# Kernel tuning notes

Hardware: AMD Instinct MI355X
Metric: run time of the kernel (lower is better)

Reference implementation:

```python
import jax, jax.numpy as jnp
import numpy as np
import math

MUL = 64
N_NODES = 20000
N_EDGES = 160000
NUM_SPECIES = 5
N_BASIS = 8
AVG_NEIGH = 8.0
SOFT_NORM_MAX = 1.0e5
# (l_in, l_filter, l_out) tensor-product paths with triangle ineq. + parity (l_in+l_f+l_out even), l_f <= 2
PATHS = [(0,0,0),(0,1,1),(0,2,2),(1,0,1),(1,1,0),(1,1,2),(1,2,1),(2,0,2),(2,1,1),(2,2,0),(2,2,2)]
SQ_PATHS = [(0,0,0),(0,1,1),(0,2,2),(1,1,0),(1,1,2),(1,2,1),(2,2,0),(2,2,2)]

def _clebsch(j1,m1,j2,m2,j3,m3):
    if m1 + m2 != m3:
        return 0.0
    f = math.factorial
    pref = math.sqrt((2*j3+1)*f(j3+j1-j2)*f(j3-j1+j2)*f(j1+j2-j3)/f(j1+j2+j3+1))
    pref *= math.sqrt(f(j3+m3)*f(j3-m3)*f(j1-m1)*f(j1+m1)*f(j2-m2)*f(j2+m2))
    s = 0.0
    for k in range(j1+j2-j3+1):
        d = [k, j1+j2-j3-k, j1-m1-k, j2+m2-k, j3-j2+m1+k, j3-j1-m2+k]
        if min(d) < 0:
            continue
        den = 1.0
        for q in d:
            den *= f(q)
        s += (-1)**k/den
    return pref*s

def _u_real(l):
    # complex->real spherical harmonic change of basis, rows = real m (-l..l)
    U = np.zeros((2*l+1, 2*l+1), dtype=np.complex128)
    U[l, l] = 1.0
    r2 = math.sqrt(2.0)
    for m in range(1, l+1):
        U[l+m, l+m] = (-1)**m/r2
        U[l+m, l-m] = 1.0/r2
        U[l-m, l-m] = 1j/r2
        U[l-m, l+m] = -1j*(-1)**m/r2
    return U

def _cg_real(l1,l2,l3):
    Cc = np.zeros((2*l1+1, 2*l2+1, 2*l3+1), dtype=np.complex128)
    for m1 in range(-l1, l1+1):
        for m2 in range(-l2, l2+1):
            m3 = m1 + m2
            if abs(m3) <= l3:
                Cc[m1+l1, m2+l2, m3+l3] = _clebsch(l1,m1,l2,m2,l3,m3)
    R = np.einsum('ai,bj,ck,ijk->abc', _u_real(l1), _u_real(l2), _u_real(l3).conj(), Cc)
    Rr, Ri = R.real, R.imag
    R = Rr if np.linalg.norm(Rr) >= np.linalg.norm(Ri) else Ri
    return jnp.asarray((R/np.linalg.norm(R)).astype(np.float32))

CG = {p: _cg_real(*p) for p in sorted(set(PATHS) | set(SQ_PATHS))}

def _sh(dirs):
    # real spherical harmonics (component normalization) of unit vectors, l=0,1,2
    x, y, z = dirs[:, 0], dirs[:, 1], dirs[:, 2]
    Y0 = jnp.ones_like(x)[:, None]
    Y1 = jnp.sqrt(3.0)*jnp.stack([y, z, x], axis=1)
    Y2 = jnp.stack([jnp.sqrt(15.0)*x*y, jnp.sqrt(15.0)*y*z,
                    jnp.sqrt(5.0)/2*(3*z*z - 1.0), jnp.sqrt(15.0)*x*z,
                    jnp.sqrt(15.0)/2*(x*x - y*y)], axis=1)
    return [Y0, Y1, Y2]

def _split(feats):
    # [.., 576] -> [[.., 64, 1], [.., 64, 3], [.., 64, 5]]
    out, s = [], 0
    for l in range(3):
        d = 2*l + 1
        out.append(feats[..., s:s+MUL*d].reshape(feats.shape[:-1] + (MUL, d)))
        s += MUL*d
    return out

def _merge(blocks):
    return jnp.concatenate([b.reshape(b.shape[:-2] + (-1,)) for b in blocks], axis=-1)

def _sus(x):
    return jnp.where(x > 0, jnp.exp(-1.0/jnp.where(x > 0, x, 1.0)), 0.0)

def _forward(vectors, node_feats, W_up, W_skip, M1, M2, M3, W_out0, W_out1, W_out2, W_down,
             node_specie, senders, receivers):
    n_node = node_feats.shape[0]
    nf = _split(node_feats)
    # self connection: species-indexed linear (skip_tp)
    Wn = W_skip[node_specie]  # [N, 3, mul, mul]
    skip = [jnp.einsum('nui,nuv->nvi', nf[l], Wn[:, l]) / np.sqrt(MUL) for l in range(3)]
    # linear_up then gather sender features
    up = [jnp.einsum('nui,uv->nvi', nf[l], W_up[l]) / np.sqrt(MUL) for l in range(3)]
    msg = [u[senders] for u in up]  # per-edge messages
    # radial MLP -> per-edge tensor-product path weights
    lengths = jnp.linalg.norm(vectors, axis=1, keepdims=True)  # [E,1]
    x = lengths[:, 0]
    safe = jnp.where(x == 0.0, 1.0, x)
    n = jnp.arange(1, N_BASIS + 1, dtype=vectors.dtype)
    bess = jnp.sqrt(2.0)*jnp.sin(jnp.pi*n*x[:, None])/safe[:, None]  # bessel, x_max=1
    env = jnp.where(x < 1.0, jnp.exp(2.0*x*x/jnp.minimum(x*x - 1.0, -1e-6)), 0.0)  # soft envelope
    r = bess * env[:, None]
    h = jax.nn.gelu(r @ M1 / np.sqrt(N_BASIS))
    h = jax.nn.gelu(h @ M2 / np.sqrt(M2.shape[0]))
    mix = h @ M3 / np.sqrt(M3.shape[0])
    mix = jnp.where(lengths == 0.0, 0.0, mix)
    w = mix.reshape(-1, len(PATHS), MUL)  # [E, n_paths, mul]
    # per-edge SH tensor product (LinearSHTP, mix=False)
    dirs = vectors / jnp.maximum(lengths, 1e-9)
    Y = _sh(dirs)
    out = [jnp.zeros_like(m) for m in msg]
    for p, (li, lf, lo) in enumerate(PATHS):
        c = jnp.einsum('eui,ej,ijk->euk', msg[li], Y[lf], CG[(li, lf, lo)])
        out[lo] = out[lo] + w[:, p, :, None]*c
    # scatter-add to receivers
    agg = [jax.ops.segment_sum(o, receivers, num_segments=n_node) / np.sqrt(AVG_NEIGH) for o in out]
    # linear_down
    dn = [jnp.einsum('nui,uv->nvi', agg[l], W_down[l]) / np.sqrt(MUL) for l in range(3)]
    # activation: gelu on even scalars, then per-mul symmetric tensor square, concat
    dn[0] = jax.nn.gelu(dn[0])
    sq = {p: jnp.einsum('nui,nuj,ijk->nuk', dn[p[0]], dn[p[1]], CG[p]) for p in SQ_PATHS}
    cat0 = jnp.concatenate([dn[0], sq[(0,0,0)], sq[(1,1,0)], sq[(2,2,0)]], axis=1)  # [N, 4*mul, 1]
    cat1 = jnp.concatenate([dn[1], sq[(0,1,1)], sq[(1,2,1)]], axis=1)               # [N, 3*mul, 3]
    cat2 = jnp.concatenate([dn[2], sq[(0,2,2)], sq[(1,1,2)], sq[(2,2,2)]], axis=1)  # [N, 4*mul, 5]
    o0 = jnp.einsum('nui,uv->nvi', cat0, W_out0) / np.sqrt(cat0.shape[1])
    o1 = jnp.einsum('nui,uv->nvi', cat1, W_out1) / np.sqrt(cat1.shape[1])
    o2 = jnp.einsum('nui,uv->nvi', cat2, W_out2) / np.sqrt(cat2.shape[1])
    # soft normalization: x * 1/(1 + (n/M)*sus(n/M))
    def sn(b):
        nrm = jnp.linalg.norm(b, axis=-1, keepdims=True) / SOFT_NORM_MAX
        return b / (1.0 + nrm*_sus(nrm))
    ob = [sn(o) for o in (o0, o1, o2)]
    final = [0.9*skip[l] + 0.45*ob[l] for l in range(3)]
    return _merge(final)  # [N, 576]

def setup_inputs() -> dict:
    key = jax.random.key(0)
    ks = jax.random.split(key, 16)
    d = jax.random.normal(ks[0], (N_EDGES, 3), dtype=jnp.float32)
    d = d / jnp.linalg.norm(d, axis=1, keepdims=True)
    lens = jax.random.uniform(ks[1], (N_EDGES, 1), minval=0.05, maxval=0.95)
    vectors = d * lens
    node_feats = jax.random.normal(ks[2], (N_NODES, MUL*9), dtype=jnp.float32)
    W_up = jax.random.normal(ks[3], (3, MUL, MUL), dtype=jnp.float32)
    W_skip = jax.random.normal(ks[4], (NUM_SPECIES, 3, MUL, MUL), dtype=jnp.float32)
    M1 = jax.random.normal(ks[5], (N_BASIS, 64), dtype=jnp.float32)
    M2 = jax.random.normal(ks[6], (64, 64), dtype=jnp.float32)
    M3 = jax.random.normal(ks[7], (64, len(PATHS)*MUL), dtype=jnp.float32)
    W_down = jax.random.normal(ks[8], (3, MUL, MUL), dtype=jnp.float32)
    W_out0 = jax.random.normal(ks[9], (4*MUL, MUL), dtype=jnp.float32)
    W_out1 = jax.random.normal(ks[10], (3*MUL, MUL), dtype=jnp.float32)
    W_out2 = jax.random.normal(ks[11], (4*MUL, MUL), dtype=jnp.float32)
    node_specie = jax.random.randint(ks[12], (N_NODES,), 0, NUM_SPECIES)
    senders = jax.random.randint(ks[13], (N_EDGES,), 0, N_NODES)
    receivers = jax.random.randint(ks[14], (N_EDGES,), 0, N_NODES)
    return {"vectors": vectors, "node_feats": node_feats, "W_up": W_up, "W_skip": W_skip,
            "M1": M1, "M2": M2, "M3": M3, "W_out0": W_out0, "W_out1": W_out1, "W_out2": W_out2,
            "W_down": W_down, "node_specie": node_specie, "senders": senders, "receivers": receivers}

def reference(vectors, node_feats, W_up, W_skip, M1, M2, M3, W_out0, W_out1, W_out2, W_down,
              node_specie, senders, receivers):
    return _forward(vectors, node_feats, W_up, W_skip, M1, M2, M3, W_out0, W_out1, W_out2, W_down,
                    node_specie, senders, receivers)
```

## Files before the change

kernel.cpp:

```cpp
#include <hip/hip_runtime.h>
#include <complex>
#include <cmath>


constexpr int NN = 20000;
constexpr int NE = 160000;

struct CGTab { float v[363]; };

static double hfact(int n){ double r=1.0; for(int i=2;i<=n;i++) r*=(double)i; return r; }
static double hcleb(int j1,int m1,int j2,int m2,int j3,int m3){
  if(m1+m2!=m3) return 0.0;
  double pref = std::sqrt((2.0*j3+1.0)*hfact(j3+j1-j2)*hfact(j3-j1+j2)*hfact(j1+j2-j3)/hfact(j1+j2+j3+1));
  pref *= std::sqrt(hfact(j3+m3)*hfact(j3-m3)*hfact(j1-m1)*hfact(j1+m1)*hfact(j2-m2)*hfact(j2+m2));
  double s=0.0;
  for(int k=0;k<=j1+j2-j3;k++){
    int d0=k,d1=j1+j2-j3-k,d2=j1-m1-k,d3=j2+m2-k,d4=j3-j2+m1+k,d5=j3-j1-m2+k;
    if(d0<0||d1<0||d2<0||d3<0||d4<0||d5<0) continue;
    double den=hfact(d0)*hfact(d1)*hfact(d2)*hfact(d3)*hfact(d4)*hfact(d5);
    s += ((k&1)?-1.0:1.0)/den;
  }
  return pref*s;
}
typedef std::complex<double> cdbl;
static void hbuildU(int l, cdbl U[5][5]){
  for(int a=0;a<5;a++)for(int b=0;b<5;b++) U[a][b]=cdbl(0.0,0.0);
  U[l][l]=cdbl(1.0,0.0);
  const double r2=std::sqrt(2.0);
  for(int m=1;m<=l;m++){
    double sgn=(m&1)?-1.0:1.0;
    U[l+m][l+m]=cdbl(sgn/r2,0.0);
    U[l+m][l-m]=cdbl(1.0/r2,0.0);
    U[l-m][l-m]=cdbl(0.0,1.0/r2);
    U[l-m][l+m]=cdbl(0.0,-sgn/r2);
  }
}
static CGTab build_cg(){
  CGTab T{};
  const int L1[11]={0,0,0,1,1,1,1,2,2,2,2};
  const int L2[11]={0,1,2,0,1,1,2,0,1,2,2};
  const int L3[11]={0,1,2,1,0,2,1,2,1,0,2};
  int off=0;
  for(int p=0;p<11;p++){
    int l1=L1[p],l2=L2[p],l3=L3[p];
    int d1=2*l1+1,d2=2*l2+1,d3=2*l3+1;
    cdbl U1[5][5],U2[5][5],U3[5][5];
    hbuildU(l1,U1); hbuildU(l2,U2); hbuildU(l3,U3);
    double Rr[125],Ri[125]; double nr=0.0,ni=0.0;
    for(int a=0;a<d1;a++)for(int b=0;b<d2;b++)for(int c=0;c<d3;c++){
      cdbl s(0.0,0.0);
      for(int i=0;i<d1;i++)for(int j=0;j<d2;j++){
        int k=(i-l1)+(j-l2)+l3;
        if(k<0||k>=d3) continue;
        double cc=hcleb(l1,i-l1,l2,j-l2,l3,k-l3);
        if(cc==0.0) continue;
        s += U1[a][i]*U2[b][j]*std::conj(U3[c][k])*cc;
      }
      int idx=(a*d2+b)*d3+c;
      Rr[idx]=s.real(); Ri[idx]=s.imag();
      nr+=s.real()*s.real(); ni+=s.imag()*s.imag();
    }
    bool useR=(nr>=ni);
    double nm=std::sqrt(useR?nr:ni);
    int sz=d1*d2*d3;
    for(int t=0;t<sz;t++) T.v[off+t]=(float)((useR?Rr[t]:Ri[t])/nm);
    off+=sz;
  }
  return T;
}
static const CGTab g_cg = build_cg();

__device__ __forceinline__ float gelu_f(float x){
  float t = tanhf(0.7978845608028654f*(x + 0.044715f*x*x*x));
  return 0.5f*x*(1.0f+t);
}

__global__ __launch_bounds__(256) void node_up_kernel(
    const float* __restrict__ nf, const float* __restrict__ Wup,
    float* __restrict__ up)
{
  __shared__ alignas(16) float NF[4][576];
  const int tid=threadIdx.x, wid=tid>>6, lane=tid&63;
  const int node=blockIdx.x*4+wid;
  float* F=NF[wid];
  const float* nr=nf+(size_t)node*576;
  #pragma unroll
  for(int t=0;t<9;t++) F[lane+t*64]=nr[lane+t*64];
  __syncthreads();
  float* ur=up+(size_t)node*576;
  {
    float a=0.f;
    for(int u4=0;u4<16;u4++){
      const float* wb=Wup+(u4*4)*64+lane;
      float w0=wb[0],w1=wb[64],w2=wb[128],w3=wb[192];
      const float4 v=*(const float4*)&F[u4*4];
      a+=v.x*w0+v.y*w1+v.z*w2+v.w*w3;
    }
    ur[lane]=a*0.125f;
  }
  {
    float a0=0.f,a1=0.f,a2=0.f;
    for(int u4=0;u4<16;u4++){
      const float* wb=Wup+4096+(u4*4)*64+lane;
      float w0=wb[0],w1=wb[64],w2=wb[128],w3=wb[192];
      const float4 A0=*(const float4*)&F[64+u4*12];
      const float4 A1=*(const float4*)&F[64+u4*12+4];
      const float4 A2=*(const float4*)&F[64+u4*12+8];
      a0 += A0.x*w0 + A0.w*w1 + A1.z*w2 + A2.y*w3;
      a1 += A0.y*w0 + A1.x*w1 + A1.w*w2 + A2.z*w3;
      a2 += A0.z*w0 + A1.y*w1 + A2.x*w2 + A2.w*w3;
    }
    ur[64+lane]=a0*0.125f; ur[128+lane]=a1*0.125f; ur[192+lane]=a2*0.125f;
  }
  {
    float a0=0.f,a1=0.f,a2=0.f,a3=0.f,a4=0.f;
    for(int u4=0;u4<16;u4++){
      const float* wb=Wup+8192+(u4*4)*64+lane;
      float w0=wb[0],w1=wb[64],w2=wb[128],w3=wb[192];
      const float4 B0=*(const float4*)&F[256+u4*20];
      const float4 B1=*(const float4*)&F[256+u4*20+4];
      const float4 B2=*(const float4*)&F[256+u4*20+8];
      const float4 B3=*(const float4*)&F[256+u4*20+12];
      const float4 B4=*(const float4*)&F[256+u4*20+16];
      a0 += B0.x*w0 + B1.y*w1 + B2.z*w2 + B3.w*w3;
      a1 += B0.y*w0 + B1.z*w1 + B2.w*w2 + B4.x*w3;
      a2 += B0.z*w0 + B1.w*w1 + B3.x*w2 + B4.y*w3;
      a3 += B0.w*w0 + B2.x*w1 + B3.y*w2 + B4.z*w3;
      a4 += B1.x*w0 + B2.y*w1 + B3.z*w2 + B4.w*w3;
    }
    ur[256+lane]=a0*0.125f; ur[320+lane]=a1*0.125f; ur[384+lane]=a2*0.125f;
    ur[448+lane]=a3*0.125f; ur[512+lane]=a4*0.125f;
  }
}

__global__ __launch_bounds__(256) void edge_kernel(
    const float* __restrict__ vectors, const int* __restrict__ senders,
    const int* __restrict__ receivers, const float* __restrict__ M1,
    const float* __restrict__ M2, const float* __restrict__ M3,
    const float* __restrict__ up, float* __restrict__ agg, CGTab cg)
{
  __shared__ alignas(16) float RL[4][64];
  __shared__ alignas(16) float HL[4][512];
  __shared__ alignas(16) float HL2[4][512];
  const int tid=threadIdx.x, wid=tid>>6, lane=tid&63;
  const int ebase=(blockIdx.x*4+wid)*8;

  {
    int el = ebase + (lane>>3);
    float vx=vectors[3*el], vy=vectors[3*el+1], vz=vectors[3*el+2];
    float xx=sqrtf(vx*vx+vy*vy+vz*vz);
    float safe=(xx==0.0f)?1.0f:xx;
    float x2=xx*xx;
    float env=(xx<1.0f)? expf(2.0f*x2/fminf(x2-1.0f,-1e-6f)) : 0.0f;
    float nb=(float)((lane&7)+1);
    RL[wid][lane] = 1.4142135623730951f*sinf(3.14159265358979f*nb*xx)/safe*env;
  }
  __syncthreads();
  {
    float m1v[8];
    #pragma unroll
    for(int b=0;b<8;b++) m1v[b]=M1[b*64+lane];
    #pragma unroll
    for(int e=0;e<8;e++){
      const float4 ra=*(const float4*)&RL[wid][e*8];
      const float4 rb=*(const float4*)&RL[wid][e*8+4];
      float acc = ra.x*m1v[0]+ra.y*m1v[1]+ra.z*m1v[2]+ra.w*m1v[3]
                + rb.x*m1v[4]+rb.y*m1v[5]+rb.z*m1v[6]+rb.w*m1v[7];
      HL[wid][e*64+lane]=gelu_f(acc*0.3535533905932738f);
    }
  }
  __syncthreads();
  {
    float h2[8]={0,0,0,0,0,0,0,0};
    for(int k4=0;k4<16;k4++){
      const float* mb=M2+(k4*4)*64+lane;
      float m2a=mb[0],m2b=mb[64],m2c=mb[128],m2d=mb[192];
      #pragma unroll
      for(int e=0;e<8;e++){
        const float4 h=*(const float4*)&HL[wid][e*64+k4*4];
        h2[e] += h.x*m2a+h.y*m2b+h.z*m2c+h.w*m2d;
      }
    }
    #pragma unroll
    for(int e=0;e<8;e++) HL2[wid][e*64+lane]=gelu_f(h2[e]*0.125f);
  }
  __syncthreads();
  float w[8][11];
  #pragma unroll
  for(int e=0;e<8;e++){
    #pragma unroll
    for(int p=0;p<11;p++) w[e][p]=0.0f;
  }
  for(int k4=0;k4<16;k4++){
    float m3v[4][11];
    #pragma unroll
    for(int q=0;q<4;q++){
      #pragma unroll
      for(int p=0;p<11;p++) m3v[q][p]=M3[(size_t)(k4*4+q)*704+p*64+lane];
    }
    #pragma unroll
    for(int e=0;e<8;e++){
      const float4 h=*(const float4*)&HL2[wid][e*64+k4*4];
      #pragma unroll
      for(int p=0;p<11;p++)
        w[e][p] += h.x*m3v[0][p]+h.y*m3v[1][p]+h.z*m3v[2][p]+h.w*m3v[3][p];
    }
  }
  #pragma unroll
  for(int e=0;e<8;e++){
    const int eid=ebase+e;
    float evx=vectors[3*eid], evy=vectors[3*eid+1], evz=vectors[3*eid+2];
    float len=sqrtf(evx*evx+evy*evy+evz*evz);
    float il=1.0f/fmaxf(len,1e-9f);
    float dx=evx*il, dy=evy*il, dz=evz*il;
    float Y1[3]={1.7320508075688772f*dy, 1.7320508075688772f*dz, 1.7320508075688772f*dx};
    float Y2[5]={3.872983346207417f*dx*dy, 3.872983346207417f*dy*dz,
                 1.118033988749895f*(3.0f*dz*dz-1.0f),
                 3.872983346207417f*dx*dz, 1.9364916731037085f*(dx*dx-dy*dy)};
    int snd=senders[eid], rcv=receivers[eid];
    const float* urow=up+(size_t)snd*576;
    float mA=urow[lane];
    float mB[3], mC[5];
    #pragma unroll
    for(int i=0;i<3;i++) mB[i]=urow[64+i*64+lane];
    #pragma unroll
    for(int i=0;i<5;i++) mC[i]=urow[256+i*64+lane];
    const float wsc=(len==0.0f)?0.0f:0.125f;
    float we[11];
    #pragma unroll
    for(int p=0;p<11;p++) we[p]=w[e][p]*wsc;
    float o0=0.0f, o1[3]={0,0,0}, o2[5]={0,0,0,0,0};
    o0 += we[0]*mA*cg.v[0];
    #pragma unroll
    for(int k=0;k<3;k++) o1[k]+= we[1]*mA*Y1[k]*cg.v[1+k*3+k];
    #pragma unroll
    for(int k=0;k<5;k++) o2[k]+= we[2]*mA*Y2[k]*cg.v[10+k*5+k];
    #pragma unroll
    for(int k=0;k<3;k++) o1[k]+= we[3]*mB[k]*cg.v[35+k*3+k];
    #pragma unroll
    for(int i=0;i<3;i++){
      float t=we[4]*mB[i];
      #pragma unroll
      for(int j=0;j<3;j++) o0 += t*Y1[j]*cg.v[44+i*3+j];
    }
    #pragma unroll
    for(int i=0;i<3;i++){
      float t=we[5]*mB[i];
      #pragma unroll
      for(int j=0;j<3;j++){
        float ty=t*Y1[j];
        #pragma unroll
        for(int k=0;k<5;k++) o2[k]+= ty*cg.v[53+(i*3+j)*5+k];
      }
    }
    #pragma unroll
    for(int i=0;i<3;i++){
      float t=we[6]*mB[i];
      #pragma unroll
      for(int j=0;j<5;j++){
        float ty=t*Y2[j];
        #pragma unroll
        for(int k=0;k<3;k++) o1[k]+= ty*cg.v[98+(i*5+j)*3+k];
      }
    }
    #pragma unroll
    for(int k=0;k<5;k++) o2[k]+= we[7]*mC[k]*cg.v[143+k*5+k];
    #pragma unroll
    for(int i=0;i<5;i++){
      float t=we[8]*mC[i];
      #pragma unroll
      for(int j=0;j<3;j++){
        float ty=t*Y1[j];
        #pragma unroll
        for(int k=0;k<3;k++) o1[k]+= ty*cg.v[168+(i*3+j)*3+k];
      }
    }
    #pragma unroll
    for(int i=0;i<5;i++){
      float t=we[9]*mC[i];
      #pragma unroll
      for(int j=0;j<5;j++) o0 += t*Y2[j]*cg.v[213+i*5+j];
    }
    #pragma unroll
    for(int i=0;i<5;i++){
      float t=we[10]*mC[i];
      #pragma unroll
      for(int j=0;j<5;j++){
        float ty=t*Y2[j];
        #pragma unroll
        for(int k=0;k<5;k++) o2[k]+= ty*cg.v[238+(i*5+j)*5+k];
      }
    }
    float* ar=agg+(size_t)rcv*576;
    const float sc=0.3535533905932738f;
    atomicAdd(ar+lane, o0*sc);
    #pragma unroll
    for(int i=0;i<3;i++) atomicAdd(ar+64+i*64+lane, o1[i]*sc);
    #pragma unroll
    for(int i=0;i<5;i++) atomicAdd(ar+256+i*64+lane, o2[i]*sc);
  }
}

__global__ __launch_bounds__(256) void final_kernel(
    const float* __restrict__ agg, const float* __restrict__ nf,
    const int* __restrict__ specie, const float* __restrict__ Wskip,
    const float* __restrict__ Wdown, const float* __restrict__ Wout0,
    const float* __restrict__ Wout1, const float* __restrict__ Wout2,
    float* __restrict__ out, CGTab cg)
{
  __shared__ alignas(16) float AG[4][576];
  __shared__ alignas(16) float NF[4][576];
  __shared__ alignas(16) float C0[4][256];
  __shared__ alignas(16) float C1[4][576];
  __shared__ alignas(16) float C2[4][1280];
  const int tid=threadIdx.x, wid=tid>>6, lane=tid&63;
  const int node=blockIdx.x*4+wid;
  float* A=AG[wid]; float* F=NF[wid];
  {
    const float* ar=agg+(size_t)node*576;
    const float* nr=nf+(size_t)node*576;
    #pragma unroll
    for(int t=0;t<9;t++){ A[lane+t*64]=ar[lane+t*64]; F[lane+t*64]=nr[lane+t*64]; }
  }
  __syncthreads();

  {
    float dn0, dn1[3], dn2[5];
    {
      float a=0.f;
      for(int u4=0;u4<16;u4++){
        const float* wb=Wdown+(u4*4)*64+lane;
        float w0=wb[0],w1=wb[64],w2=wb[128],w3=wb[192];
        const float4 v=*(const float4*)&A[u4*4];
        a+=v.x*w0+v.y*w1+v.z*w2+v.w*w3;
      }
      dn0=gelu_f(a*0.125f);
    }
    {
      float a0=0.f,a1=0.f,a2=0.f;
      for(int u4=0;u4<16;u4++){
        const float* wb=Wdown+4096+(u4*4)*64+lane;
        float w0=wb[0],w1=wb[64],w2=wb[128],w3=wb[192];
        const float4 v0=*(const float4*)&A[64+u4*4];
        const float4 v1=*(const float4*)&A[128+u4*4];
        const float4 v2=*(const float4*)&A[192+u4*4];
        a0+=v0.x*w0+v0.y*w1+v0.z*w2+v0.w*w3;
        a1+=v1.x*w0+v1.y*w1+v1.z*w2+v1.w*w3;
        a2+=v2.x*w0+v2.y*w1+v2.z*w2+v2.w*w3;
      }
      dn1[0]=a0*0.125f; dn1[1]=a1*0.125f; dn1[2]=a2*0.125f;
    }
    {
      float a[5]={0,0,0,0,0};
      for(int u4=0;u4<16;u4++){
        const float* wb=Wdown+8192+(u4*4)*64+lane;
        float w0=wb[0],w1=wb[64],w2=wb[128],w3=wb[192];
        #pragma unroll
        for(int i=0;i<5;i++){
          const float4 v=*(const float4*)&A[256+i*64+u4*4];
          a[i]+=v.x*w0+v.y*w1+v.z*w2+v.w*w3;
        }
      }
      #pragma unroll
      for(int i=0;i<5;i++) dn2[i]=a[i]*0.125f;
    }
    float* c0=C0[wid]; float* c1=C1[wid]; float* c2=C2[wid];
    c0[lane]=dn0;
    c0[64+lane]=dn0*dn0*cg.v[0];
    { float s=0.f;
      #pragma unroll
      for(int i=0;i<3;i++){
        #pragma unroll
        for(int j=0;j<3;j++) s+=dn1[i]*dn1[j]*cg.v[44+i*3+j];
      }
      c0[128+lane]=s;
    }
    { float s=0.f;
      #pragma unroll
      for(int i=0;i<5;i++){
        #pragma unroll
        for(int j=0;j<5;j++) s+=dn2[i]*dn2[j]*cg.v[213+i*5+j];
      }
      c0[192+lane]=s;
    }
    #pragma unroll
    for(int i=0;i<3;i++){
      c1[i*192+lane]=dn1[i];
      c1[i*192+64+lane]=dn0*dn1[i]*cg.v[1+i*3+i];
    }
    { float s[3]={0,0,0};
      #pragma unroll
      for(int i=0;i<3;i++){
        #pragma unroll
        for(int j=0;j<5;j++){
          float t=dn1[i]*dn2[j];
          #pragma unroll
          for(int k=0;k<3;k++) s[k]+=t*cg.v[98+(i*5+j)*3+k];
        }
      }
      #pragma unroll
      for(int k=0;k<3;k++) c1[k*192+128+lane]=s[k];
    }
    #pragma unroll
    for(int i=0;i<5;i++){
      c2[i*256+lane]=dn2[i];
      c2[i*256+64+lane]=dn0*dn2[i]*cg.v[10+i*5+i];
    }
    { float s[5]={0,0,0,0,0};
      #pragma unroll
      for(int i=0;i<3;i++){
        #pragma unroll
        for(int j=0;j<3;j++){
          float t=dn1[i]*dn1[j];
          #pragma unroll
          for(int k=0;k<5;k++) s[k]+=t*cg.v[53+(i*3+j)*5+k];
        }
      }
      #pragma unroll
      for(int k=0;k<5;k++) c2[k*256+128+lane]=s[k];
    }
    { float s[5]={0,0,0,0,0};
      #pragma unroll
      for(int i=0;i<5;i++){
        #pragma unroll
        for(int j=0;j<5;j++){
          float t=dn2[i]*dn2[j];
          #pragma unroll
          for(int k=0;k<5;k++) s[k]+=t*cg.v[238+(i*5+j)*5+k];
        }
      }
      #pragma unroll
      for(int k=0;k<5;k++) c2[k*256+192+lane]=s[k];
    }
  }
  __syncthreads();

  {
    float o0=0.f;
    const float* CC=C0[wid];
    for(int u4=0;u4<64;u4++){
      const float* wb=Wout0+(u4*4)*64+lane;
      float w0=wb[0],w1=wb[64],w2=wb[128],w3=wb[192];
      const float4 v=*(const float4*)&CC[u4*4];
      o0+=v.x*w0+v.y*w1+v.z*w2+v.w*w3;
    }
    o0*=0.0625f;
    float n=fabsf(o0)*1e-5f;
    float s=(n>0.0f)?expf(-1.0f/n):0.0f;
    A[lane]=0.45f*o0/(1.0f+n*s);
  }
  {
    float o1[3]={0,0,0};
    const float* CC=C1[wid];
    for(int u4=0;u4<48;u4++){
      const float* wb=Wout1+(u4*4)*64+lane;
      float w0=wb[0],w1=wb[64],w2=wb[128],w3=wb[192];
      #pragma unroll
      for(int i=0;i<3;i++){
        const float4 v=*(const float4*)&CC[i*192+u4*4];
        o1[i]+=v.x*w0+v.y*w1+v.z*w2+v.w*w3;
      }
    }
    #pragma unroll
    for(int i=0;i<3;i++) o1[i]*=0.07216878364870323f;
    float n=sqrtf(o1[0]*o1[0]+o1[1]*o1[1]+o1[2]*o1[2])*1e-5f;
    float s=(n>0.0f)?expf(-1.0f/n):0.0f;
    float f1=0.45f/(1.0f+n*s);
    #pragma unroll
    for(int i=0;i<3;i++) A[64+lane*3+i]=o1[i]*f1;
  }
  {
    float o2[5]={0,0,0,0,0};
    const float* CC=C2[wid];
    for(int u4=0;u4<64;u4++){
      const float* wb=Wout2+(u4*4)*64+lane;
      float w0=wb[0],w1=wb[64],w2=wb[128],w3=wb[192];
      #pragma unroll
      for(int i=0;i<5;i++){
        const float4 v=*(const float4*)&CC[i*256+u4*4];
        o2[i]+=v.x*w0+v.y*w1+v.z*w2+v.w*w3;
      }
    }
    #pragma unroll
    for(int i=0;i<5;i++) o2[i]*=0.0625f;
    float n=sqrtf(o2[0]*o2[0]+o2[1]*o2[1]+o2[2]*o2[2]+o2[3]*o2[3]+o2[4]*o2[4])*1e-5f;
    float s=(n>0.0f)?expf(-1.0f/n):0.0f;
    float f2=0.45f/(1.0f+n*s);
    #pragma unroll
    for(int i=0;i<5;i++) A[256+lane*5+i]=o2[i]*f2;
  }

  const int sp=specie[node];
  const float* Ws=Wskip+(size_t)sp*12288;
  {
    float a=0.f;
    for(int u4=0;u4<16;u4++){
      const float* wb=Ws+(u4*4)*64+lane;
      float w0=wb[0],w1=wb[64],w2=wb[128],w3=wb[192];
      const float4 v=*(const float4*)&F[u4*4];
      a+=v.x*w0+v.y*w1+v.z*w2+v.w*w3;
    }
    A[lane]+=0.1125f*a;
  }
  {
    float a0=0.f,a1=0.f,a2=0.f;
    for(int u4=0;u4<16;u4++){
      const float* wb=Ws+4096+(u4*4)*64+lane;
      float w0=wb[0],w1=wb[64],w2=wb[128],w3=wb[192];
      const float4 A0=*(const float4*)&F[64+u4*12];
      const float4 A1=*(const float4*)&F[64+u4*12+4];
      const float4 A2=*(const float4*)&F[64+u4*12+8];
      a0 += A0.x*w0 + A0.w*w1 + A1.z*w2 + A2.y*w3;
      a1 += A0.y*w0 + A1.x*w1 + A1.w*w2 + A2.z*w3;
      a2 += A0.z*w0 + A1.y*w1 + A2.x*w2 + A2.w*w3;
    }
    A[64+lane*3+0]+=0.1125f*a0;
    A[64+lane*3+1]+=0.1125f*a1;
    A[64+lane*3+2]+=0.1125f*a2;
  }
  {
    float a0=0.f,a1=0.f,a2=0.f,a3=0.f,a4=0.f;
    for(int u4=0;u4<16;u4++){
      const float* wb=Ws+8192+(u4*4)*64+lane;
      float w0=wb[0],w1=wb[64],w2=wb[128],w3=wb[192];
      const float4 B0=*(const float4*)&F[256+u4*20];
      const float4 B1=*(const float4*)&F[256+u4*20+4];
      const float4 B2=*(const float4*)&F[256+u4*20+8];
      const float4 B3=*(const float4*)&F[256+u4*20+12];
      const float4 B4=*(const float4*)&F[256+u4*20+16];
      a0 += B0.x*w0 + B1.y*w1 + B2.z*w2 + B3.w*w3;
      a1 += B0.y*w0 + B1.z*w1 + B2.w*w2 + B4.x*w3;
      a2 += B0.z*w0 + B1.w*w1 + B3.x*w2 + B4.y*w3;
      a3 += B0.w*w0 + B2.x*w1 + B3.y*w2 + B4.z*w3;
      a4 += B1.x*w0 + B2.y*w1 + B3.z*w2 + B4.w*w3;
    }
    A[256+lane*5+0]+=0.1125f*a0;
    A[256+lane*5+1]+=0.1125f*a1;
    A[256+lane*5+2]+=0.1125f*a2;
    A[256+lane*5+3]+=0.1125f*a3;
    A[256+lane*5+4]+=0.1125f*a4;
  }
  __syncthreads();
  float* orow=out+(size_t)node*576;
  #pragma unroll
  for(int t=0;t<9;t++) orow[lane+t*64]=A[lane+t*64];
}

extern "C" void kernel_launch(void* const* d_in, const int* in_sizes, int n_in,
                              void* d_out, int out_size, void* d_ws, size_t ws_size,
                              hipStream_t stream) {
  (void)in_sizes; (void)n_in; (void)out_size; (void)ws_size;
  const float* vectors    =(const float*)d_in[0];
  const float* node_feats =(const float*)d_in[1];
  const float* W_up       =(const float*)d_in[2];
  const float* W_skip     =(const float*)d_in[3];
  const float* M1         =(const float*)d_in[4];
  const float* M2         =(const float*)d_in[5];
  const float* M3         =(const float*)d_in[6];
  const float* W_out0     =(const float*)d_in[7];
  const float* W_out1     =(const float*)d_in[8];
  const float* W_out2     =(const float*)d_in[9];
  const float* W_down     =(const float*)d_in[10];
  const int*   node_specie=(const int*)d_in[11];
  const int*   senders    =(const int*)d_in[12];
  const int*   receivers  =(const int*)d_in[13];
  float* out=(float*)d_out;
  float* ws=(float*)d_ws;
  float* up  = ws;
  float* agg = ws + (size_t)NN*576;

  hipMemsetAsync(agg, 0, (size_t)NN*576*sizeof(float), stream);
  node_up_kernel<<<NN/4, 256, 0, stream>>>(node_feats, W_up, up);
  edge_kernel<<<NE/32, 256, 0, stream>>>(vectors, senders, receivers,
                                         M1, M2, M3, up, agg, g_cg);
  final_kernel<<<NN/4, 256, 0, stream>>>(agg, node_feats, node_specie, W_skip,
                                         W_down, W_out0, W_out1, W_out2, out, g_cg);
}
```

Before: 1.271 ms.

## Split edge kernel into MLP and tensor-product kernels with bf16 chunked intermediate

The fused edge kernel is split into an MLP kernel, which computes the per-edge radial weights and stores them as bf16, and a tensor-product kernel that reads those weights and scatters into agg. The work runs in chunks of 32000 edges, and the chunk buffer reuses the output array as scratch. The M3 contraction is done in two halves to cut register pressure, and the launch bounds ask for more waves per SIMD. The cost is an extra global round trip, a loss of precision from bf16 weights, and a dependence on the output buffer being large enough to hold the scratch.

```diff
diff --git a/kernel.cpp b/kernel.cpp
--- a/kernel.cpp
+++ b/kernel.cpp
@@ -1,10 +1,12 @@
 #include <hip/hip_runtime.h>
+#include <hip/hip_bf16.h>
 #include <complex>
 #include <cmath>
 
 
 constexpr int NN = 20000;
 constexpr int NE = 160000;
+constexpr int ECH = 32000;
 
 struct CGTab { float v[363]; };
 
@@ -133,17 +135,51 @@
   }
 }
 
-__global__ __launch_bounds__(256) void edge_kernel(
-    const float* __restrict__ vectors, const int* __restrict__ senders,
-    const int* __restrict__ receivers, const float* __restrict__ M1,
+template<int P0,int NP>
+__device__ __forceinline__ void m3_half(
+    const float* __restrict__ M3, const float* __restrict__ hl2,
+    __hip_bfloat16* __restrict__ mix, int ebase_local, int lane)
+{
+  float w[8][NP];
+  #pragma unroll
+  for(int e=0;e<8;e++){
+    #pragma unroll
+    for(int p=0;p<NP;p++) w[e][p]=0.0f;
+  }
+  for(int k4=0;k4<16;k4++){
+    float m3v[4][NP];
+    #pragma unroll
+    for(int q=0;q<4;q++){
+      #pragma unroll
+      for(int p=0;p<NP;p++) m3v[q][p]=M3[(size_t)(k4*4+q)*704+(P0+p)*64+lane];
+    }
+    #pragma unroll
+    for(int e=0;e<8;e++){
+      const float4 h=*(const float4*)&hl2[e*64+k4*4];
+      #pragma unroll
+      for(int p=0;p<NP;p++)
+        w[e][p] += h.x*m3v[0][p]+h.y*m3v[1][p]+h.z*m3v[2][p]+h.w*m3v[3][p];
+    }
+  }
+  #pragma unroll
+  for(int e=0;e<8;e++){
+    #pragma unroll
+    for(int p=0;p<NP;p++)
+      mix[(size_t)(ebase_local+e)*704+(P0+p)*64+lane]=__float2bfloat16(w[e][p]);
+  }
+}
+
+__global__ __launch_bounds__(256,3) void mlp_kernel(
+    const float* __restrict__ vectors, const float* __restrict__ M1,
     const float* __restrict__ M2, const float* __restrict__ M3,
-    const float* __restrict__ up, float* __restrict__ agg, CGTab cg)
+    __hip_bfloat16* __restrict__ mix, int e0)
 {
   __shared__ alignas(16) float RL[4][64];
   __shared__ alignas(16) float HL[4][512];
   __shared__ alignas(16) float HL2[4][512];
   const int tid=threadIdx.x, wid=tid>>6, lane=tid&63;
-  const int ebase=(blockIdx.x*4+wid)*8;
+  const int ebase_local=(blockIdx.x*4+wid)*8;
+  const int ebase=e0+ebase_local;
 
   {
     int el = ebase + (lane>>3);
@@ -182,33 +218,24 @@
       }
     }
     #pragma unroll
-    for(int e=0;e<8;e++) HL2[wid][e*64+lane]=gelu_f(h2[e]*0.125f);
+    for(int e=0;e<8;e++) HL2[wid][e*64+lane]=gelu_f(h2[e]*0.125f)*0.125f;
   }
   __syncthreads();
-  float w[8][11];
-  #pragma unroll
+  m3_half<0,6>(M3, HL2[wid], mix, ebase_local, lane);
+  m3_half<6,5>(M3, HL2[wid], mix, ebase_local, lane);
+}
+
+__global__ __launch_bounds__(256,4) void tp_kernel(
+    const float* __restrict__ vectors, const int* __restrict__ senders,
+    const int* __restrict__ receivers, const __hip_bfloat16* __restrict__ mix,
+    const float* __restrict__ up, float* __restrict__ agg, int e0, CGTab cg)
+{
+  const int tid=threadIdx.x, wid=tid>>6, lane=tid&63;
+  const int ebase_local=(blockIdx.x*4+wid)*8;
+  #pragma unroll 2
   for(int e=0;e<8;e++){
-    #pragma unroll
-    for(int p=0;p<11;p++) w[e][p]=0.0f;
-  }
-  for(int k4=0;k4<16;k4++){
-    float m3v[4][11];
-    #pragma unroll
-    for(int q=0;q<4;q++){
-      #pragma unroll
-      for(int p=0;p<11;p++) m3v[q][p]=M3[(size_t)(k4*4+q)*704+p*64+lane];
-    }
-    #pragma unroll
-    for(int e=0;e<8;e++){
-      const float4 h=*(const float4*)&HL2[wid][e*64+k4*4];
-      #pragma unroll
-      for(int p=0;p<11;p++)
-        w[e][p] += h.x*m3v[0][p]+h.y*m3v[1][p]+h.z*m3v[2][p]+h.w*m3v[3][p];
-    }
-  }
-  #pragma unroll
-  for(int e=0;e<8;e++){
-    const int eid=ebase+e;
+    const int elocal=ebase_local+e;
+    const int eid=e0+elocal;
     float evx=vectors[3*eid], evy=vectors[3*eid+1], evz=vectors[3*eid+2];
     float len=sqrtf(evx*evx+evy*evy+evz*evz);
     float il=1.0f/fmaxf(len,1e-9f);
@@ -217,6 +244,11 @@
     float Y2[5]={3.872983346207417f*dx*dy, 3.872983346207417f*dy*dz,
                  1.118033988749895f*(3.0f*dz*dz-1.0f),
                  3.872983346207417f*dx*dz, 1.9364916731037085f*(dx*dx-dy*dy)};
+    const float zm=(len==0.0f)?0.0f:1.0f;
+    const __hip_bfloat16* wr=mix+(size_t)elocal*704;
+    float we[11];
+    #pragma unroll
+    for(int p=0;p<11;p++) we[p]=__bfloat162float(wr[p*64+lane])*zm;
     int snd=senders[eid], rcv=receivers[eid];
     const float* urow=up+(size_t)snd*576;
     float mA=urow[lane];
@@ -225,10 +257,6 @@
     for(int i=0;i<3;i++) mB[i]=urow[64+i*64+lane];
     #pragma unroll
     for(int i=0;i<5;i++) mC[i]=urow[256+i*64+lane];
-    const float wsc=(len==0.0f)?0.0f:0.125f;
-    float we[11];
-    #pragma unroll
-    for(int p=0;p<11;p++) we[p]=w[e][p]*wsc;
     float o0=0.0f, o1[3]={0,0,0}, o2[5]={0,0,0,0,0};
     o0 += we[0]*mA*cg.v[0];
     #pragma unroll
@@ -568,11 +596,15 @@
   float* ws=(float*)d_ws;
   float* up  = ws;
   float* agg = ws + (size_t)NN*576;
+  __hip_bfloat16* mix = (__hip_bfloat16*)d_out;
 
   hipMemsetAsync(agg, 0, (size_t)NN*576*sizeof(float), stream);
   node_up_kernel<<<NN/4, 256, 0, stream>>>(node_feats, W_up, up);
-  edge_kernel<<<NE/32, 256, 0, stream>>>(vectors, senders, receivers,
-                                         M1, M2, M3, up, agg, g_cg);
+  for(int e0=0; e0<NE; e0+=ECH){
+    mlp_kernel<<<ECH/32, 256, 0, stream>>>(vectors, M1, M2, M3, mix, e0);
+    tp_kernel<<<ECH/32, 256, 0, stream>>>(vectors, senders, receivers,
+                                          mix, up, agg, e0, g_cg);
+  }
   final_kernel<<<NN/4, 256, 0, stream>>>(agg, node_feats, node_specie, W_skip,
                                          W_down, W_out0, W_out1, W_out2, out, g_cg);
 }
```

Result: slower. 1.991 ms (+56.7%).
